# Optimization experiments

Hardware: AMD Instinct MI355X
Metric: run time of the kernel (lower is better)

The kernel has to match this reference:

```python
import jax, jax.numpy as jnp
from jax import lax
import numpy as np

_B, _D, _H, _W = 4, 32, 256, 256   # batch, sparse grid (z,y,x)
_NPER = 50000                      # active voxels per batch element
_EPS = 1e-3                        # BatchNorm eps from norm_fn


def _subm_rulebook(coords, D, H, W):
    # gather/scatter index pairs for a 3x3x3 submanifold conv (spconv rulebook)
    N = coords.shape[0]
    b, z, y, x = coords.T
    keys = ((b * D + z) * H + y) * W + x
    order = np.argsort(keys)
    sk = keys[order]
    rin, rout = [], []
    for dz in (-1, 0, 1):
        for dy in (-1, 0, 1):
            for dx in (-1, 0, 1):
                nz, ny, nx = z + dz, y + dy, x + dx
                valid = (nz >= 0) & (nz < D) & (ny >= 0) & (ny < H) & (nx >= 0) & (nx < W)
                qk = ((b * D + nz) * H + ny) * W + nx
                pos = np.clip(np.searchsorted(sk, qk), 0, N - 1)
                found = valid & (sk[pos] == qk)
                rin.append(order[pos[found]].astype(np.int32))
                rout.append(np.nonzero(found)[0].astype(np.int32))
    P = max(len(a) for a in rin)
    Ia = np.full((27, P), N, np.int32)   # sentinel N -> zero-padded row
    Oa = np.full((27, P), N, np.int32)
    for k in range(27):
        Ia[k, :len(rin[k])] = rin[k]
        Oa[k, :len(rout[k])] = rout[k]
    return Ia, Oa


def _build():
    rng = np.random.default_rng(0)
    coords = []
    for b in range(_B):
        lin = rng.choice(_D * _H * _W, _NPER, replace=False)
        z = lin // (_H * _W); y = (lin // _W) % _H; x = lin % _W
        coords.append(np.stack([np.full(_NPER, b), z, y, x], 1))
    coords = np.concatenate(coords).astype(np.int64)
    N = coords.shape[0]
    rb1_in, rb1_out = _subm_rulebook(coords, _D, _H, _W)
    # strided SparseConv3d (k=3, s=2, p=1) rulebook + output coord set
    Do, Ho, Wo = (_D - 1) // 2 + 1, (_H - 1) // 2 + 1, (_W - 1) // 2 + 1
    b, z, y, x = coords.T
    cin, ck, ckey = [], [], []
    k = 0
    for dz in range(3):
        for dy in range(3):
            for dx in range(3):
                oz2, oy2, ox2 = z + 1 - dz, y + 1 - dy, x + 1 - dx
                valid = (oz2 % 2 == 0) & (oy2 % 2 == 0) & (ox2 % 2 == 0)
                oz, oy, ox = oz2 // 2, oy2 // 2, ox2 // 2
                valid &= (oz >= 0) & (oz < Do) & (oy >= 0) & (oy < Ho) & (ox >= 0) & (ox < Wo)
                idx = np.nonzero(valid)[0]
                cin.append(idx)
                ck.append(np.full(len(idx), k))
                ckey.append(((b[idx] * Do + oz[idx]) * Ho + oy[idx]) * Wo + ox[idx])
                k += 1
    allkey = np.concatenate(ckey)
    ukeys, inv = np.unique(allkey, return_inverse=True)
    N2 = len(ukeys)
    cin = np.concatenate(cin); ck = np.concatenate(ck)
    Pd = max(int((ck == kk).sum()) for kk in range(27))
    Id = np.full((27, Pd), N, np.int32)
    Od = np.full((27, Pd), N2, np.int32)
    for kk in range(27):
        m = ck == kk; n = int(m.sum())
        Id[kk, :n] = cin[m]; Od[kk, :n] = inv[m]
    ox = ukeys % Wo; oy = (ukeys // Wo) % Ho
    oz = (ukeys // (Wo * Ho)) % Do; ob = ukeys // (Wo * Ho * Do)
    coords2 = np.stack([ob, oz, oy, ox], 1)
    rb2_in, rb2_out = _subm_rulebook(coords2, Do, Ho, Wo)
    return N, N2, rb1_in, rb1_out, Id, Od, rb2_in, rb2_out


def setup_inputs():
    N, N2, rb1_in, rb1_out, rbd_in, rbd_out, rb2_in, rb2_out = _build()
    ks = jax.random.split(jax.random.key(0), 8)
    Cin, C0, C1 = 5, 16, 32
    return dict(
        voxel_features=jax.random.normal(ks[0], (N, Cin), jnp.float32),
        W_in=jax.random.normal(ks[1], (27, Cin, C0), jnp.float32) * 0.1,
        g_in=jnp.ones(C0), b_in=jnp.zeros(C0),
        Wb1=jax.random.normal(ks[2], (2, 2, 27, C0, C0), jnp.float32) * 0.05,
        bb1=jnp.zeros((2, 2, C0)), gb1=jnp.ones((2, 2, C0)), beb1=jnp.zeros((2, 2, C0)),
        Wp=jax.random.normal(ks[3], (27, C0, 1), jnp.float32) * 0.05,
        Wd=jax.random.normal(ks[4], (27, C0, C1), jnp.float32) * 0.05,
        g_d=jnp.ones(C1), b_d=jnp.zeros(C1),
        Wb2=jax.random.normal(ks[5], (2, 2, 27, C1, C1), jnp.float32) * 0.05,
        bb2=jnp.zeros((2, 2, C1)), gb2=jnp.ones((2, 2, C1)), beb2=jnp.zeros((2, 2, C1)),
        rb1_in=jnp.asarray(rb1_in), rb1_out=jnp.asarray(rb1_out),
        rbd_in=jnp.asarray(rbd_in), rbd_out=jnp.asarray(rbd_out),
        rb2_in=jnp.asarray(rb2_in), rb2_out=jnp.asarray(rb2_out),
        n2=int(N2),
    )


def _sparse_conv(feat, W, rin, rout, nout):
    # rulebook gather-matmul-scatter; fixed 27-iteration loop over kernel offsets
    featp = jnp.concatenate([feat, jnp.zeros((1, feat.shape[1]), feat.dtype)], 0)
    out = jnp.zeros((nout + 1, W.shape[-1]), feat.dtype)
    for k in range(W.shape[0]):
        out = out.at[rout[k]].add(featp[rin[k]] @ W[k])
    return out[:nout]


def _bn(x, g, b):
    # training-mode BatchNorm1d over active voxels (eps=1e-3)
    m = x.mean(0)
    v = ((x - m) ** 2).mean(0)
    return g * (x - m) * lax.rsqrt(v + _EPS) + b


def _basic_block(feat, Wb, bb, gb, beb, rin, rout, n):
    out = _sparse_conv(feat, Wb[0], rin, rout, n) + bb[0]
    out = jax.nn.relu(_bn(out, gb[0], beb[0]))
    out = _sparse_conv(out, Wb[1], rin, rout, n) + bb[1]
    out = _bn(out, gb[1], beb[1])
    return jax.nn.relu(out + feat)


def _forward(voxel_features, W_in, g_in, b_in, Wb1, bb1, gb1, beb1, Wp, Wd, g_d, b_d,
             Wb2, bb2, gb2, beb2, rb1_in, rb1_out, rbd_in, rbd_out, rb2_in, rb2_out, n2):
    n1 = voxel_features.shape[0]
    # conv_input: SubMConv3d + BN + ReLU
    x = jax.nn.relu(_bn(_sparse_conv(voxel_features, W_in, rb1_in, rb1_out, n1), g_in, b_in))
    for i in range(2):
        x = _basic_block(x, Wb1[i], bb1[i], gb1[i], beb1[i], rb1_in, rb1_out, n1)
    # DynamicFocalPruningDownsample: learnable importance -> topk keep (1-0.5)
    imp = jax.nn.sigmoid(_sparse_conv(x, Wp, rb1_in, rb1_out, n1))[:, 0]
    x = x * imp[:, None]
    kkeep = n1 - n1 // 2
    kth = lax.top_k(imp, kkeep)[0][-1]
    x = jnp.where(imp[:, None] >= kth, x, jnp.zeros_like(x))
    # strided SparseConv3d 16->32 + BN + ReLU
    x2 = jax.nn.relu(_bn(_sparse_conv(x, Wd, rbd_in, rbd_out, n2), g_d, b_d))
    for i in range(2):
        x2 = _basic_block(x2, Wb2[i], bb2[i], gb2[i], beb2[i], rb2_in, rb2_out, n2)
    return x2


def reference(voxel_features, W_in, g_in, b_in, Wb1, bb1, gb1, beb1, Wp, Wd, g_d, b_d,
              Wb2, bb2, gb2, beb2, rb1_in, rb1_out, rbd_in, rbd_out, rb2_in, rb2_out, n2):
    return _forward(voxel_features, W_in, g_in, b_in, Wb1, bb1, gb1, beb1, Wp, Wd, g_d, b_d,
                    Wb2, bb2, gb2, beb2, rb1_in, rb1_out, rbd_in, rbd_out, rb2_in, rb2_out, n2)
```

## Files before the change

kernel.cpp:

```cpp
#include <hip/hip_runtime.h>


typedef __attribute__((ext_vector_type(8))) short bf16x8;
typedef __attribute__((ext_vector_type(4))) float f32x4;

static __device__ __forceinline__ unsigned f2bfu(float x) {
    unsigned b = __float_as_uint(x);
    return (b + 0x7FFFu + ((b >> 16) & 1u)) >> 16;
}

__global__ void rb_count_kernel(const int* __restrict__ rout, int P, int n_out,
                                int* __restrict__ cnt) {
    int k = threadIdx.x;
    if (k >= 27) return;
    const int* r = rout + (size_t)k * P;
    int lo = 0, hi = P;
    while (lo < hi) {
        int mid = (lo + hi) >> 1;
        if (r[mid] < n_out) lo = mid + 1; else hi = mid;
    }
    cnt[k] = lo;
}

__global__ void seg_build(const int* __restrict__ rout, const int* __restrict__ cnt,
                          int P, int nb, int gran, int* __restrict__ segs) {
    const int k = blockIdx.y;
    const int b = blockIdx.x * 256 + threadIdx.x;
    if (b > nb) return;
    const int target = b * gran;
    const int* r = rout + (size_t)k * P;
    int lo = 0, hi = cnt[k];
    while (lo < hi) {
        int m = (lo + hi) >> 1;
        if (r[m] < target) lo = m + 1; else hi = m;
    }
    segs[k * (nb + 1) + b] = lo;
}

__global__ void inv_build(const int* __restrict__ rin, const int* __restrict__ rout,
                          const int* __restrict__ cnt, int P, int n_out,
                          int* __restrict__ inv) {
    const int k = blockIdx.y;
    const int p = blockIdx.x * 256 + threadIdx.x;
    if (p < cnt[k])
        inv[(size_t)k * n_out + rout[(size_t)k * P + p]] = rin[(size_t)k * P + p];
}

__global__ void prepack_w(const float* __restrict__ W, int T, int CI, int S,
                          short* __restrict__ pack) {
    int idx = blockIdx.x * 256 + threadIdx.x;
    if (idx >= S * 128) return;
    int l = idx & 63, h = (idx >> 6) & 1, s = idx >> 7;
    int co = (l & 15) + 16 * h;
#pragma unroll
    for (int j = 0; j < 8; j++) {
        int gk = s * 32 + (l >> 4) * 8 + j;
        int tap = gk / CI, cin = gk % CI;
        float w = (tap < T) ? W[((size_t)tap * CI + cin) * 32 + co] : 0.f;
        pack[(size_t)idx * 8 + j] = (short)f2bfu(w);
    }
}

__global__ __launch_bounds__(256) void conv_mfma_sorted32(
        const float* __restrict__ feat, const short* __restrict__ Bp,
        const int* __restrict__ rin, const int* __restrict__ rout,
        const int* __restrict__ segs, int P, int nb16, int n_out,
        float* __restrict__ out, float* __restrict__ stats) {
    __shared__ int invw[64];
    __shared__ float part[2][4][32];
    const int t = threadIdx.x, wv = t >> 6, lane = t & 63;
    const int row = lane & 15, grp = lane >> 4;
    float ss0 = 0.f, qq0 = 0.f, ss1 = 0.f, qq1 = 0.f;

    for (int tile = 0; tile < 4; ++tile) {
        const int rowbase = blockIdx.x * 256 + wv * 64 + tile * 16;
        if (rowbase >= n_out) break;
        const int tix = rowbase >> 4;
        int segv = 0;
        if (lane < 28)      segv = segs[lane * (nb16 + 1) + tix];
        else if (lane < 56) segv = segs[(lane - 28) * (nb16 + 1) + tix + 1];
        f32x4 d0 = {0.f, 0.f, 0.f, 0.f}, d1 = {0.f, 0.f, 0.f, 0.f};
        for (int k = 0; k < 27; ++k) {
            const int s0 = __shfl(segv, k);
            const int s1 = __shfl(segv, 28 + k);
            if (s0 == s1) continue;
            if (lane < 16) invw[wv * 16 + lane] = -1;
            const int e = s0 + lane;
            if (lane < 16 && e < s1)
                invw[wv * 16 + (rout[(size_t)k * P + e] - rowbase)] = rin[(size_t)k * P + e];
            asm volatile("s_waitcnt lgkmcnt(0)" ::: "memory");
            const int rn = invw[wv * 16 + row];
            unsigned au0 = 0, au1 = 0, au2 = 0, au3 = 0;
            if (rn >= 0) {
                const float4 v0 = *(const float4*)(feat + (size_t)rn * 32 + grp * 8);
                const float4 v1 = *(const float4*)(feat + (size_t)rn * 32 + grp * 8 + 4);
                au0 = f2bfu(v0.x) | (f2bfu(v0.y) << 16);
                au1 = f2bfu(v0.z) | (f2bfu(v0.w) << 16);
                au2 = f2bfu(v1.x) | (f2bfu(v1.y) << 16);
                au3 = f2bfu(v1.z) | (f2bfu(v1.w) << 16);
            }
            union { unsigned u[4]; bf16x8 v; } ua;
            ua.u[0] = au0; ua.u[1] = au1; ua.u[2] = au2; ua.u[3] = au3;
            const bf16x8 b0 = *(const bf16x8*)(Bp + ((size_t)(2 * k) * 64 + lane) * 8);
            const bf16x8 b1 = *(const bf16x8*)(Bp + ((size_t)(2 * k + 1) * 64 + lane) * 8);
            d0 = __builtin_amdgcn_mfma_f32_16x16x32_bf16(ua.v, b0, d0, 0, 0, 0);
            d1 = __builtin_amdgcn_mfma_f32_16x16x32_bf16(ua.v, b1, d1, 0, 0, 0);
        }
        const int m0 = rowbase + grp * 4;
#pragma unroll
        for (int i = 0; i < 4; i++) {
            if (m0 + i < n_out) {
                out[(size_t)(m0 + i) * 32 + row]      = d0[i];
                out[(size_t)(m0 + i) * 32 + row + 16] = d1[i];
            }
            ss0 += d0[i]; qq0 += d0[i] * d0[i];
            ss1 += d1[i]; qq1 += d1[i] * d1[i];
        }
    }
#pragma unroll
    for (int d = 16; d <= 32; d <<= 1) {
        ss0 += __shfl_xor(ss0, d); qq0 += __shfl_xor(qq0, d);
        ss1 += __shfl_xor(ss1, d); qq1 += __shfl_xor(qq1, d);
    }
    if (lane < 16) {
        part[0][wv][row] = ss0; part[0][wv][row + 16] = ss1;
        part[1][wv][row] = qq0; part[1][wv][row + 16] = qq1;
    }
    __syncthreads();
    if (t < 64) {
        const int which = t >> 5, co = t & 31;
        atomicAdd(&stats[which * 32 + co],
                  part[which][0][co] + part[which][1][co] +
                  part[which][2][co] + part[which][3][co]);
    }
}

__global__ __launch_bounds__(256) void conv_mfma_inv16(
        const float* __restrict__ feat, const short* __restrict__ Bp,
        const int* __restrict__ inv, int n_out,
        float* __restrict__ out, float* __restrict__ stats) {
    __shared__ float part[2][4][32];
    const int t = threadIdx.x, wv = t >> 6, lane = t & 63;
    const int row = lane & 15, grp = lane >> 4;
    float ss0 = 0.f, qq0 = 0.f, ss1 = 0.f, qq1 = 0.f;

    for (int tile = 0; tile < 4; ++tile) {
        const int rowbase = blockIdx.x * 256 + wv * 64 + tile * 16;
        if (rowbase >= n_out) break;
        const int j = rowbase + row;
        f32x4 d0 = {0.f, 0.f, 0.f, 0.f}, d1 = {0.f, 0.f, 0.f, 0.f};
        for (int s = 0; s < 14; ++s) {
            const int tap = 2 * s + (grp >> 1);
            const int cin0 = (grp & 1) * 8;
            int rn = -1;
            if (tap < 27 && j < n_out) rn = inv[(size_t)tap * n_out + j];
            unsigned au0 = 0, au1 = 0, au2 = 0, au3 = 0;
            if (rn >= 0) {
                const float4 v0 = *(const float4*)(feat + (size_t)rn * 16 + cin0);
                const float4 v1 = *(const float4*)(feat + (size_t)rn * 16 + cin0 + 4);
                au0 = f2bfu(v0.x) | (f2bfu(v0.y) << 16);
                au1 = f2bfu(v0.z) | (f2bfu(v0.w) << 16);
                au2 = f2bfu(v1.x) | (f2bfu(v1.y) << 16);
                au3 = f2bfu(v1.z) | (f2bfu(v1.w) << 16);
            }
            union { unsigned u[4]; bf16x8 v; } ua;
            ua.u[0] = au0; ua.u[1] = au1; ua.u[2] = au2; ua.u[3] = au3;
            const bf16x8 b0 = *(const bf16x8*)(Bp + ((size_t)(2 * s) * 64 + lane) * 8);
            const bf16x8 b1 = *(const bf16x8*)(Bp + ((size_t)(2 * s + 1) * 64 + lane) * 8);
            d0 = __builtin_amdgcn_mfma_f32_16x16x32_bf16(ua.v, b0, d0, 0, 0, 0);
            d1 = __builtin_amdgcn_mfma_f32_16x16x32_bf16(ua.v, b1, d1, 0, 0, 0);
        }
        const int m0 = rowbase + grp * 4;
#pragma unroll
        for (int i = 0; i < 4; i++) {
            if (m0 + i < n_out) {
                out[(size_t)(m0 + i) * 32 + row]      = d0[i];
                out[(size_t)(m0 + i) * 32 + row + 16] = d1[i];
            }
            ss0 += d0[i]; qq0 += d0[i] * d0[i];
            ss1 += d1[i]; qq1 += d1[i] * d1[i];
        }
    }
#pragma unroll
    for (int d = 16; d <= 32; d <<= 1) {
        ss0 += __shfl_xor(ss0, d); qq0 += __shfl_xor(qq0, d);
        ss1 += __shfl_xor(ss1, d); qq1 += __shfl_xor(qq1, d);
    }
    if (lane < 16) {
        part[0][wv][row] = ss0; part[0][wv][row + 16] = ss1;
        part[1][wv][row] = qq0; part[1][wv][row + 16] = qq1;
    }
    __syncthreads();
    if (t < 64) {
        const int which = t >> 5, co = t & 31;
        atomicAdd(&stats[which * 32 + co],
                  part[which][0][co] + part[which][1][co] +
                  part[which][2][co] + part[which][3][co]);
    }
}

template <int COUT, bool SIGMOID, bool STATS>
__global__ __launch_bounds__(256) void conv16_wave(
        const float* __restrict__ feat, const float* __restrict__ W,
        const int* __restrict__ rin, const int* __restrict__ rout,
        const int* __restrict__ segs, int P, int nb64, int n_out,
        float* __restrict__ out, float* __restrict__ stats) {
    __shared__ int invw[4 * 64];
    __shared__ float part[2][4][COUT];
    const int t = threadIdx.x, wv = t >> 6, lane = t & 63;
    const int rowbase = blockIdx.x * 256 + wv * 64;
    const bool active = rowbase < n_out;
    float acc[COUT];
#pragma unroll
    for (int co = 0; co < COUT; co++) acc[co] = 0.f;

    if (active) {
        const int tix = rowbase >> 6;
        int segv = 0;
        if (lane < 28)      segv = segs[lane * (nb64 + 1) + tix];
        else if (lane < 56) segv = segs[(lane - 28) * (nb64 + 1) + tix + 1];
        for (int k = 0; k < 27; ++k) {
            const int s0 = __shfl(segv, k);
            const int s1 = __shfl(segv, 28 + k);
            if (s0 == s1) continue;
            invw[wv * 64 + lane] = -1;
            const int e = s0 + lane;
            if (e < s1)
                invw[wv * 64 + (rout[(size_t)k * P + e] - rowbase)] = rin[(size_t)k * P + e];
            asm volatile("s_waitcnt lgkmcnt(0)" ::: "memory");
            const int rn = invw[wv * 64 + lane];
            float f[16];
#pragma unroll
            for (int ci = 0; ci < 16; ci++) f[ci] = 0.f;
            if (rn >= 0) {
                const float* fr = feat + (size_t)rn * 16;
#pragma unroll
                for (int q = 0; q < 4; q++) {
                    const float4 v = *(const float4*)(fr + 4 * q);
                    f[4 * q] = v.x; f[4 * q + 1] = v.y;
                    f[4 * q + 2] = v.z; f[4 * q + 3] = v.w;
                }
            }
            const float* __restrict__ Wk = W + k * 16 * COUT;
#pragma unroll
            for (int ci = 0; ci < 16; ci++) {
                const float fv = f[ci];
#pragma unroll
                for (int co = 0; co < COUT; co++)
                    acc[co] = fmaf(fv, Wk[ci * COUT + co], acc[co]);
            }
        }
        const int j = rowbase + lane;
        if (j < n_out) {
#pragma unroll
            for (int co = 0; co < COUT; co++) {
                float v = acc[co];
                if (SIGMOID) v = 1.f / (1.f + expf(-v));
                out[(size_t)j * COUT + co] = v;
            }
        }
    }
    if (STATS) {
#pragma unroll
        for (int co = 0; co < COUT; co++) {
            float s = acc[co], s2 = s * s;
#pragma unroll
            for (int d = 1; d < 64; d <<= 1) {
                s += __shfl_xor(s, d);
                s2 += __shfl_xor(s2, d);
            }
            if (lane == 0) { part[0][wv][co] = s; part[1][wv][co] = s2; }
        }
        __syncthreads();
        if (t < 2 * COUT) {
            const int which = t / COUT, co = t - which * COUT;
            atomicAdd(&stats[which * COUT + co],
                      part[which][0][co] + part[which][1][co] +
                      part[which][2][co] + part[which][3][co]);
        }
    }
}

template <int CIN, int COUT>
__global__ __launch_bounds__(256) void conv_gather(
        const float* __restrict__ feat, const float* __restrict__ W,
        const int* __restrict__ rin, const int* __restrict__ rout,
        const int* __restrict__ segs, int P, int n_out,
        float* __restrict__ out, float* __restrict__ stats) {
    __shared__ int2 invl[256];
    __shared__ int seg[54];
    __shared__ float part[2][4][COUT];
    const int t = threadIdx.x;
    const int j0 = blockIdx.x * 256;
    const int nb1 = gridDim.x + 1;
    if (t < 54) seg[t] = segs[(t >> 1) * nb1 + blockIdx.x + (t & 1)];
    invl[t] = make_int2(-1, -1);
    float acc[COUT];
#pragma unroll
    for (int co = 0; co < COUT; co++) acc[co] = 0.f;
    __syncthreads();

    for (int k = 0; k < 27; k++) {
        const int s0 = seg[2 * k], s1 = seg[2 * k + 1];
        if (s0 == s1) continue;
        const int idx = s0 + t;
        if (idx < s1)
            invl[rout[(size_t)k * P + idx] - j0] = make_int2(k, rin[(size_t)k * P + idx]);
        __syncthreads();
        const int2 e = invl[t];
        const int in = (e.x == k) ? e.y : -1;
        __syncthreads();

        float f[CIN];
#pragma unroll
        for (int ci = 0; ci < CIN; ci++) f[ci] = 0.f;
        if (in >= 0) {
            const float* fr = feat + (size_t)in * CIN;
#pragma unroll
            for (int ci = 0; ci < CIN; ci++) f[ci] = fr[ci];
        }
        const float* __restrict__ Wk = W + k * CIN * COUT;
#pragma unroll
        for (int ci = 0; ci < CIN; ci++) {
            const float fv = f[ci];
#pragma unroll
            for (int co = 0; co < COUT; co++)
                acc[co] = fmaf(fv, Wk[ci * COUT + co], acc[co]);
        }
    }

    const int j = j0 + t;
    if (j < n_out) {
#pragma unroll
        for (int co = 0; co < COUT; co++) out[(size_t)j * COUT + co] = acc[co];
    }
    const int wv = t >> 6, lane = t & 63;
#pragma unroll
    for (int co = 0; co < COUT; co++) {
        float s = acc[co], s2 = s * s;
#pragma unroll
        for (int d = 1; d < 64; d <<= 1) {
            s += __shfl_xor(s, d);
            s2 += __shfl_xor(s2, d);
        }
        if (lane == 0) { part[0][wv][co] = s; part[1][wv][co] = s2; }
    }
    __syncthreads();
    if (t < 2 * COUT) {
        const int which = t / COUT, co = t - which * COUT;
        atomicAdd(&stats[which * COUT + co],
                  part[which][0][co] + part[which][1][co] +
                  part[which][2][co] + part[which][3][co]);
    }
}

template <int C, bool RELU>
__global__ void bn_apply(const float* __restrict__ x, const float* __restrict__ stats,
                         const float* __restrict__ gg, const float* __restrict__ bb,
                         int n, float* __restrict__ y) {
    const float nf = (float)n;
    const long long total = (long long)n * C;
    for (long long idx = (long long)blockIdx.x * blockDim.x + threadIdx.x;
         idx < total; idx += (long long)gridDim.x * blockDim.x) {
        int ch = (int)(idx & (C - 1));
        float m = stats[ch] / nf;
        float v = stats[C + ch] / nf - m * m;
        float r = rsqrtf(v + 1e-3f);
        float val = gg[ch] * (x[idx] - m) * r + bb[ch];
        if (RELU) val = fmaxf(val, 0.f);
        y[idx] = val;
    }
}

template <int C>
__global__ void bn_apply_addrelu(const float* __restrict__ x,
                                 const float* __restrict__ skip,
                                 const float* __restrict__ stats,
                                 const float* __restrict__ gg,
                                 const float* __restrict__ bb,
                                 int n, float* __restrict__ y) {
    const float nf = (float)n;
    const long long total = (long long)n * C;
    for (long long idx = (long long)blockIdx.x * blockDim.x + threadIdx.x;
         idx < total; idx += (long long)gridDim.x * blockDim.x) {
        int ch = (int)(idx & (C - 1));
        float m = stats[ch] / nf;
        float v = stats[C + ch] / nf - m * m;
        float r = rsqrtf(v + 1e-3f);
        float val = gg[ch] * (x[idx] - m) * r + bb[ch] + skip[idx];
        y[idx] = fmaxf(val, 0.f);
    }
}

__global__ __launch_bounds__(256) void hist_pass(const float* __restrict__ imp, int n,
                                                 int pass, const int* __restrict__ state,
                                                 int* __restrict__ hist) {
    __shared__ int lh[256];
    const int t = threadIdx.x;
    lh[t] = 0;
    __syncthreads();
    const int shift = 24 - 8 * pass;
    unsigned prefix = 0;
    if (pass > 0) prefix = (unsigned)state[0];
    for (int i = blockIdx.x * 256 + t; i < n; i += gridDim.x * 256) {
        unsigned u = __float_as_uint(imp[i]);
        if (pass == 0 || (u >> (shift + 8)) == prefix)
            atomicAdd(&lh[(u >> shift) & 0xFFu], 1);
    }
    __syncthreads();
    if (lh[t]) atomicAdd(&hist[pass * 256 + t], lh[t]);
}

__global__ __launch_bounds__(256) void scan_byte(const int* __restrict__ hist,
                                                 int kkeep, int pass,
                                                 int* __restrict__ state) {
    __shared__ int h[256];
    const int t = threadIdx.x;
    h[t] = hist[pass * 256 + t];
    __syncthreads();
    if (t == 0) {
        const int target = (pass == 0) ? kkeep : state[1];
        int acc = 0; int b = 255;
        for (; b > 0; b--) {
            if (acc + h[b] >= target) break;
            acc += h[b];
        }
        unsigned prefix = (pass == 0) ? 0u : (unsigned)state[0];
        prefix = (prefix << 8) | (unsigned)b;
        state[0] = (int)prefix;
        state[1] = target - acc;
        if (pass == 3) state[2] = (int)prefix;
    }
}

__global__ void prune_mask(float* __restrict__ x, const float* __restrict__ imp,
                           const int* __restrict__ state, int n) {
    const unsigned K = (unsigned)state[2];
    int i = blockIdx.x * blockDim.x + threadIdx.x;
    if (i >= n) return;
    float im = imp[i];
    float mult = (__float_as_uint(im) >= K) ? im : 0.f;
#pragma unroll
    for (int c = 0; c < 16; c++) x[(size_t)i * 16 + c] *= mult;
}

extern "C" void kernel_launch(void* const* d_in, const int* in_sizes, int n_in,
                              void* d_out, int out_size, void* d_ws, size_t ws_size,
                              hipStream_t stream) {
    const float* vf    = (const float*)d_in[0];
    const float* W_in  = (const float*)d_in[1];
    const float* g_in  = (const float*)d_in[2];
    const float* b_in  = (const float*)d_in[3];
    const float* Wb1   = (const float*)d_in[4];
    const float* gb1   = (const float*)d_in[6];
    const float* beb1  = (const float*)d_in[7];
    const float* Wp    = (const float*)d_in[8];
    const float* Wd    = (const float*)d_in[9];
    const float* g_d   = (const float*)d_in[10];
    const float* b_d   = (const float*)d_in[11];
    const float* Wb2   = (const float*)d_in[12];
    const float* gb2   = (const float*)d_in[14];
    const float* beb2  = (const float*)d_in[15];
    const int* rb1_in  = (const int*)d_in[16];
    const int* rb1_out = (const int*)d_in[17];
    const int* rbd_in  = (const int*)d_in[18];
    const int* rbd_out = (const int*)d_in[19];
    const int* rb2_in  = (const int*)d_in[20];
    const int* rb2_out = (const int*)d_in[21];

    const int N  = in_sizes[0] / 5;
    const int P1 = in_sizes[16] / 27;
    const int Pd = in_sizes[18] / 27;
    const int P2 = in_sizes[20] / 27;
    const int n2 = out_size / 32;
    const int kkeep = N - N / 2;

    const int gs1   = (N + 255) / 256;
    const int gm2   = (n2 + 255) / 256;
    const int nb16  = (n2 + 15) / 16;
    const int nb64  = (N + 63) / 64;
    const int gew   = 2048;

    auto pad4 = [](size_t v) { return (v + 3) & ~(size_t)3; };
    float* A     = (float*)d_ws;
    float* B     = A   + pad4((size_t)N * 16);
    float* imp   = B   + pad4((size_t)N * 16);
    float* D     = imp + pad4((size_t)N);
    float* E     = D   + pad4((size_t)n2 * 32);
    float* stats = E   + pad4((size_t)n2 * 32);
    int*   cnt1  = (int*)(stats + 64);
    int*   cntd  = cnt1 + 32;
    int*   cnt2  = cntd + 32;
    int*   hist4 = cnt2 + 32;
    int*   state = hist4 + 1024;
    int*   segs1 = state + 8;
    int*   segs64 = segs1 + 27 * (gs1 + 1);
    int*   invd   = (int*)E;
    int*   segs16 = (int*)B;
    short* pack2  = (short*)imp;
    short* packd  = pack2 + 4 * 27648;
    float* OUT   = (float*)d_out;
    float* C2    = OUT;

    rb_count_kernel<<<1, 32, 0, stream>>>(rb1_out, P1, N,  cnt1);
    rb_count_kernel<<<1, 32, 0, stream>>>(rbd_out, Pd, n2, cntd);
    rb_count_kernel<<<1, 32, 0, stream>>>(rb2_out, P2, n2, cnt2);
    seg_build<<<dim3((gs1 + 256) / 256, 27), 256, 0, stream>>>(rb1_out, cnt1, P1, gs1, 256, segs1);
    seg_build<<<dim3((nb64 + 256) / 256, 27), 256, 0, stream>>>(rb1_out, cnt1, P1, nb64, 64, segs64);

    hipMemsetAsync(stats, 0, 64 * 4, stream);
    conv_gather<5, 16><<<gs1, 256, 0, stream>>>(vf, W_in, rb1_in, rb1_out, segs1, P1, N, B, stats);
    bn_apply<16, true><<<gew, 256, 0, stream>>>(B, stats, g_in, b_in, N, A);

    for (int i = 0; i < 2; i++) {
        const float* W0 = Wb1 + (size_t)(i * 2 + 0) * 27 * 256;
        const float* W1 = Wb1 + (size_t)(i * 2 + 1) * 27 * 256;
        hipMemsetAsync(stats, 0, 64 * 4, stream);
        conv16_wave<16, false, true><<<gs1, 256, 0, stream>>>(A, W0, rb1_in, rb1_out, segs64, P1, nb64, N, B, stats);
        bn_apply<16, true><<<gew, 256, 0, stream>>>(B, stats, gb1 + (i * 2 + 0) * 16, beb1 + (i * 2 + 0) * 16, N, B);
        hipMemsetAsync(stats, 0, 64 * 4, stream);
        conv16_wave<16, false, true><<<gs1, 256, 0, stream>>>(B, W1, rb1_in, rb1_out, segs64, P1, nb64, N, C2, stats);
        bn_apply_addrelu<16><<<gew, 256, 0, stream>>>(C2, A, stats, gb1 + (i * 2 + 1) * 16, beb1 + (i * 2 + 1) * 16, N, A);
    }

    conv16_wave<1, true, false><<<gs1, 256, 0, stream>>>(A, Wp, rb1_in, rb1_out, segs64, P1, nb64, N, imp, stats);
    hipMemsetAsync(hist4, 0, 1024 * 4, stream);
    for (int p = 0; p < 4; p++) {
        hist_pass<<<128, 256, 0, stream>>>(imp, N, p, state, hist4);
        scan_byte<<<1, 256, 0, stream>>>(hist4, kkeep, p, state);
    }
    prune_mask<<<(N + 255) / 256, 256, 0, stream>>>(A, imp, state, N);

    seg_build<<<dim3((nb16 + 256) / 256, 27), 256, 0, stream>>>(rb2_out, cnt2, P2, nb16, 16, segs16);
    for (int w = 0; w < 4; w++)
        prepack_w<<<14, 256, 0, stream>>>(Wb2 + (size_t)w * 27 * 1024, 27, 32, 27, pack2 + (size_t)w * 27648);
    prepack_w<<<7, 256, 0, stream>>>(Wd, 27, 16, 14, packd);
    hipMemsetAsync(invd, 0xFF, (size_t)27 * n2 * 4, stream);
    inv_build<<<dim3((Pd + 255) / 256, 27), 256, 0, stream>>>(rbd_in, rbd_out, cntd, Pd, n2, invd);

    hipMemsetAsync(stats, 0, 64 * 4, stream);
    conv_mfma_inv16<<<gm2, 256, 0, stream>>>(A, packd, invd, n2, D, stats);
    bn_apply<32, true><<<gew, 256, 0, stream>>>(D, stats, g_d, b_d, n2, D);

    for (int i = 0; i < 2; i++) {
        const short* P0 = pack2 + (size_t)(i * 2 + 0) * 27648;
        const short* P1w = pack2 + (size_t)(i * 2 + 1) * 27648;
        hipMemsetAsync(stats, 0, 64 * 4, stream);
        conv_mfma_sorted32<<<gm2, 256, 0, stream>>>(D, P0, rb2_in, rb2_out, segs16, P2, nb16, n2, E, stats);
        bn_apply<32, true><<<gew, 256, 0, stream>>>(E, stats, gb2 + (i * 2 + 0) * 32, beb2 + (i * 2 + 0) * 32, n2, E);
        hipMemsetAsync(stats, 0, 64 * 4, stream);
        conv_mfma_sorted32<<<gm2, 256, 0, stream>>>(E, P1w, rb2_in, rb2_out, segs16, P2, nb16, n2, OUT, stats);
        bn_apply_addrelu<32><<<gew, 256, 0, stream>>>(OUT, D, stats, gb2 + (i * 2 + 1) * 32, beb2 + (i * 2 + 1) * 32, n2, (i == 0) ? D : OUT);
    }
}
```

Baseline: 1.522 ms.

## Store stage-2 activations in bf16 and swizzle block order across XCDs

After: 1.282 ms. -15.8%, faster.

```diff
diff --git a/kernel.cpp b/kernel.cpp
--- a/kernel.cpp
+++ b/kernel.cpp
@@ -7,6 +7,15 @@
 static __device__ __forceinline__ unsigned f2bfu(float x) {
     unsigned b = __float_as_uint(x);
     return (b + 0x7FFFu + ((b >> 16) & 1u)) >> 16;
+}
+static __device__ __forceinline__ float bf2f(unsigned short u) {
+    return __uint_as_float(((unsigned)u) << 16);
+}
+static __device__ __forceinline__ int xcd_swz(int bid, int nwg) {
+    if (nwg < 16) return bid;
+    int q = nwg >> 3, r = nwg & 7;
+    int x = bid & 7, i = bid >> 3;
+    return (x < r ? x * (q + 1) : r * (q + 1) + (x - r) * q) + i;
 }
 
 __global__ void rb_count_kernel(const int* __restrict__ rout, int P, int n_out,
@@ -61,19 +70,21 @@
     }
 }
 
+template <bool OUT_BF16>
 __global__ __launch_bounds__(256) void conv_mfma_sorted32(
-        const float* __restrict__ feat, const short* __restrict__ Bp,
+        const unsigned short* __restrict__ feat, const short* __restrict__ Bp,
         const int* __restrict__ rin, const int* __restrict__ rout,
         const int* __restrict__ segs, int P, int nb16, int n_out,
-        float* __restrict__ out, float* __restrict__ stats) {
+        void* __restrict__ outv, float* __restrict__ stats) {
     __shared__ int invw[64];
     __shared__ float part[2][4][32];
     const int t = threadIdx.x, wv = t >> 6, lane = t & 63;
     const int row = lane & 15, grp = lane >> 4;
+    const int bid = xcd_swz(blockIdx.x, gridDim.x);
     float ss0 = 0.f, qq0 = 0.f, ss1 = 0.f, qq1 = 0.f;
 
     for (int tile = 0; tile < 4; ++tile) {
-        const int rowbase = blockIdx.x * 256 + wv * 64 + tile * 16;
+        const int rowbase = bid * 256 + wv * 64 + tile * 16;
         if (rowbase >= n_out) break;
         const int tix = rowbase >> 4;
         int segv = 0;
@@ -90,17 +101,10 @@
                 invw[wv * 16 + (rout[(size_t)k * P + e] - rowbase)] = rin[(size_t)k * P + e];
             asm volatile("s_waitcnt lgkmcnt(0)" ::: "memory");
             const int rn = invw[wv * 16 + row];
-            unsigned au0 = 0, au1 = 0, au2 = 0, au3 = 0;
-            if (rn >= 0) {
-                const float4 v0 = *(const float4*)(feat + (size_t)rn * 32 + grp * 8);
-                const float4 v1 = *(const float4*)(feat + (size_t)rn * 32 + grp * 8 + 4);
-                au0 = f2bfu(v0.x) | (f2bfu(v0.y) << 16);
-                au1 = f2bfu(v0.z) | (f2bfu(v0.w) << 16);
-                au2 = f2bfu(v1.x) | (f2bfu(v1.y) << 16);
-                au3 = f2bfu(v1.z) | (f2bfu(v1.w) << 16);
-            }
-            union { unsigned u[4]; bf16x8 v; } ua;
-            ua.u[0] = au0; ua.u[1] = au1; ua.u[2] = au2; ua.u[3] = au3;
+            union { int u[4]; bf16x8 v; } ua;
+            ua.u[0] = ua.u[1] = ua.u[2] = ua.u[3] = 0;
+            if (rn >= 0)
+                ua.v = *(const bf16x8*)(feat + (size_t)rn * 32 + grp * 8);
             const bf16x8 b0 = *(const bf16x8*)(Bp + ((size_t)(2 * k) * 64 + lane) * 8);
             const bf16x8 b1 = *(const bf16x8*)(Bp + ((size_t)(2 * k + 1) * 64 + lane) * 8);
             d0 = __builtin_amdgcn_mfma_f32_16x16x32_bf16(ua.v, b0, d0, 0, 0, 0);
@@ -110,8 +114,15 @@
 #pragma unroll
         for (int i = 0; i < 4; i++) {
             if (m0 + i < n_out) {
-                out[(size_t)(m0 + i) * 32 + row]      = d0[i];
-                out[(size_t)(m0 + i) * 32 + row + 16] = d1[i];
+                if (OUT_BF16) {
+                    unsigned short* o = (unsigned short*)outv;
+                    o[(size_t)(m0 + i) * 32 + row]      = (unsigned short)f2bfu(d0[i]);
+                    o[(size_t)(m0 + i) * 32 + row + 16] = (unsigned short)f2bfu(d1[i]);
+                } else {
+                    float* o = (float*)outv;
+                    o[(size_t)(m0 + i) * 32 + row]      = d0[i];
+                    o[(size_t)(m0 + i) * 32 + row + 16] = d1[i];
+                }
             }
             ss0 += d0[i]; qq0 += d0[i] * d0[i];
             ss1 += d1[i]; qq1 += d1[i] * d1[i];
@@ -136,16 +147,17 @@
 }
 
 __global__ __launch_bounds__(256) void conv_mfma_inv16(
-        const float* __restrict__ feat, const short* __restrict__ Bp,
+        const unsigned short* __restrict__ feat, const short* __restrict__ Bp,
         const int* __restrict__ inv, int n_out,
-        float* __restrict__ out, float* __restrict__ stats) {
+        unsigned short* __restrict__ out, float* __restrict__ stats) {
     __shared__ float part[2][4][32];
     const int t = threadIdx.x, wv = t >> 6, lane = t & 63;
     const int row = lane & 15, grp = lane >> 4;
+    const int bid = xcd_swz(blockIdx.x, gridDim.x);
     float ss0 = 0.f, qq0 = 0.f, ss1 = 0.f, qq1 = 0.f;
 
     for (int tile = 0; tile < 4; ++tile) {
-        const int rowbase = blockIdx.x * 256 + wv * 64 + tile * 16;
+        const int rowbase = bid * 256 + wv * 64 + tile * 16;
         if (rowbase >= n_out) break;
         const int j = rowbase + row;
         f32x4 d0 = {0.f, 0.f, 0.f, 0.f}, d1 = {0.f, 0.f, 0.f, 0.f};
@@ -154,17 +166,10 @@
             const int cin0 = (grp & 1) * 8;
             int rn = -1;
             if (tap < 27 && j < n_out) rn = inv[(size_t)tap * n_out + j];
-            unsigned au0 = 0, au1 = 0, au2 = 0, au3 = 0;
-            if (rn >= 0) {
-                const float4 v0 = *(const float4*)(feat + (size_t)rn * 16 + cin0);
-                const float4 v1 = *(const float4*)(feat + (size_t)rn * 16 + cin0 + 4);
-                au0 = f2bfu(v0.x) | (f2bfu(v0.y) << 16);
-                au1 = f2bfu(v0.z) | (f2bfu(v0.w) << 16);
-                au2 = f2bfu(v1.x) | (f2bfu(v1.y) << 16);
-                au3 = f2bfu(v1.z) | (f2bfu(v1.w) << 16);
-            }
-            union { unsigned u[4]; bf16x8 v; } ua;
-            ua.u[0] = au0; ua.u[1] = au1; ua.u[2] = au2; ua.u[3] = au3;
+            union { int u[4]; bf16x8 v; } ua;
+            ua.u[0] = ua.u[1] = ua.u[2] = ua.u[3] = 0;
+            if (rn >= 0)
+                ua.v = *(const bf16x8*)(feat + (size_t)rn * 16 + cin0);
             const bf16x8 b0 = *(const bf16x8*)(Bp + ((size_t)(2 * s) * 64 + lane) * 8);
             const bf16x8 b1 = *(const bf16x8*)(Bp + ((size_t)(2 * s + 1) * 64 + lane) * 8);
             d0 = __builtin_amdgcn_mfma_f32_16x16x32_bf16(ua.v, b0, d0, 0, 0, 0);
@@ -174,8 +179,8 @@
 #pragma unroll
         for (int i = 0; i < 4; i++) {
             if (m0 + i < n_out) {
-                out[(size_t)(m0 + i) * 32 + row]      = d0[i];
-                out[(size_t)(m0 + i) * 32 + row + 16] = d1[i];
+                out[(size_t)(m0 + i) * 32 + row]      = (unsigned short)f2bfu(d0[i]);
+                out[(size_t)(m0 + i) * 32 + row + 16] = (unsigned short)f2bfu(d1[i]);
             }
             ss0 += d0[i]; qq0 += d0[i] * d0[i];
             ss1 += d1[i]; qq1 += d1[i] * d1[i];
@@ -208,7 +213,8 @@
     __shared__ int invw[4 * 64];
     __shared__ float part[2][4][COUT];
     const int t = threadIdx.x, wv = t >> 6, lane = t & 63;
-    const int rowbase = blockIdx.x * 256 + wv * 64;
+    const int bid = xcd_swz(blockIdx.x, gridDim.x);
+    const int rowbase = bid * 256 + wv * 64;
     const bool active = rowbase < n_out;
     float acc[COUT];
 #pragma unroll
@@ -291,9 +297,10 @@
     __shared__ int seg[54];
     __shared__ float part[2][4][COUT];
     const int t = threadIdx.x;
-    const int j0 = blockIdx.x * 256;
+    const int bid = xcd_swz(blockIdx.x, gridDim.x);
+    const int j0 = bid * 256;
     const int nb1 = gridDim.x + 1;
-    if (t < 54) seg[t] = segs[(t >> 1) * nb1 + blockIdx.x + (t & 1)];
+    if (t < 54) seg[t] = segs[(t >> 1) * nb1 + bid + (t & 1)];
     invl[t] = make_int2(-1, -1);
     float acc[COUT];
 #pragma unroll
@@ -392,6 +399,47 @@
     }
 }
 
+template <int C>
+__global__ void bn_apply_b(const unsigned short* __restrict__ x,
+                           const float* __restrict__ stats,
+                           const float* __restrict__ gg, const float* __restrict__ bb,
+                           int n, unsigned short* __restrict__ y) {
+    const float nf = (float)n;
+    const long long total = (long long)n * C;
+    for (long long idx = (long long)blockIdx.x * blockDim.x + threadIdx.x;
+         idx < total; idx += (long long)gridDim.x * blockDim.x) {
+        int ch = (int)(idx & (C - 1));
+        float m = stats[ch] / nf;
+        float v = stats[C + ch] / nf - m * m;
+        float r = rsqrtf(v + 1e-3f);
+        float val = gg[ch] * (bf2f(x[idx]) - m) * r + bb[ch];
+        val = fmaxf(val, 0.f);
+        y[idx] = (unsigned short)f2bfu(val);
+    }
+}
+
+template <int C, bool OUT_BF16>
+__global__ void bn_addrelu_sb(const float* __restrict__ x,
+                              const unsigned short* __restrict__ skip,
+                              const float* __restrict__ stats,
+                              const float* __restrict__ gg,
+                              const float* __restrict__ bb,
+                              int n, void* __restrict__ yv) {
+    const float nf = (float)n;
+    const long long total = (long long)n * C;
+    for (long long idx = (long long)blockIdx.x * blockDim.x + threadIdx.x;
+         idx < total; idx += (long long)gridDim.x * blockDim.x) {
+        int ch = (int)(idx & (C - 1));
+        float m = stats[ch] / nf;
+        float v = stats[C + ch] / nf - m * m;
+        float r = rsqrtf(v + 1e-3f);
+        float val = gg[ch] * (x[idx] - m) * r + bb[ch] + bf2f(skip[idx]);
+        val = fmaxf(val, 0.f);
+        if (OUT_BF16) ((unsigned short*)yv)[idx] = (unsigned short)f2bfu(val);
+        else          ((float*)yv)[idx] = val;
+    }
+}
+
 __global__ __launch_bounds__(256) void hist_pass(const float* __restrict__ imp, int n,
                                                  int pass, const int* __restrict__ state,
                                                  int* __restrict__ hist) {
@@ -433,15 +481,17 @@
     }
 }
 
-__global__ void prune_mask(float* __restrict__ x, const float* __restrict__ imp,
-                           const int* __restrict__ state, int n) {
+__global__ void prune_mask_ab(const float* __restrict__ x, const float* __restrict__ imp,
+                              const int* __restrict__ state, int n,
+                              unsigned short* __restrict__ ab) {
     const unsigned K = (unsigned)state[2];
     int i = blockIdx.x * blockDim.x + threadIdx.x;
     if (i >= n) return;
     float im = imp[i];
     float mult = (__float_as_uint(im) >= K) ? im : 0.f;
 #pragma unroll
-    for (int c = 0; c < 16; c++) x[(size_t)i * 16 + c] *= mult;
+    for (int c = 0; c < 16; c++)
+        ab[(size_t)i * 16 + c] = (unsigned short)f2bfu(x[(size_t)i * 16 + c] * mult);
 }
 
 extern "C" void kernel_launch(void* const* d_in, const int* in_sizes, int n_in,
@@ -485,9 +535,10 @@
     float* A     = (float*)d_ws;
     float* B     = A   + pad4((size_t)N * 16);
     float* imp   = B   + pad4((size_t)N * 16);
-    float* D     = imp + pad4((size_t)N);
-    float* E     = D   + pad4((size_t)n2 * 32);
-    float* stats = E   + pad4((size_t)n2 * 32);
+    float* FI    = imp + pad4((size_t)N);
+    float* Dbf   = FI  + pad4((size_t)n2 * 32);
+    float* Ebf   = Dbf + pad4((size_t)n2 * 16);
+    float* stats = Ebf + pad4((size_t)n2 * 16);
     int*   cnt1  = (int*)(stats + 64);
     int*   cntd  = cnt1 + 32;
     int*   cnt2  = cntd + 32;
@@ -495,10 +546,14 @@
     int*   state = hist4 + 1024;
     int*   segs1 = state + 8;
     int*   segs64 = segs1 + 27 * (gs1 + 1);
-    int*   invd   = (int*)E;
-    int*   segs16 = (int*)B;
+    int*   invd   = (int*)FI;
+    float* F      = FI;
+    unsigned short* Ab = (unsigned short*)B;
+    int*   segs16 = (int*)(B + pad4((size_t)N * 8));
     short* pack2  = (short*)imp;
     short* packd  = pack2 + 4 * 27648;
+    unsigned short* Db = (unsigned short*)Dbf;
+    unsigned short* Eb = (unsigned short*)Ebf;
     float* OUT   = (float*)d_out;
     float* C2    = OUT;
 
@@ -529,7 +584,7 @@
         hist_pass<<<128, 256, 0, stream>>>(imp, N, p, state, hist4);
         scan_byte<<<1, 256, 0, stream>>>(hist4, kkeep, p, state);
     }
-    prune_mask<<<(N + 255) / 256, 256, 0, stream>>>(A, imp, state, N);
+    prune_mask_ab<<<(N + 255) / 256, 256, 0, stream>>>(A, imp, state, N, Ab);
 
     seg_build<<<dim3((nb16 + 256) / 256, 27), 256, 0, stream>>>(rb2_out, cnt2, P2, nb16, 16, segs16);
     for (int w = 0; w < 4; w++)
@@ -539,17 +594,20 @@
     inv_build<<<dim3((Pd + 255) / 256, 27), 256, 0, stream>>>(rbd_in, rbd_out, cntd, Pd, n2, invd);
 
     hipMemsetAsync(stats, 0, 64 * 4, stream);
-    conv_mfma_inv16<<<gm2, 256, 0, stream>>>(A, packd, invd, n2, D, stats);
-    bn_apply<32, true><<<gew, 256, 0, stream>>>(D, stats, g_d, b_d, n2, D);
+    conv_mfma_inv16<<<gm2, 256, 0, stream>>>(Ab, packd, invd, n2, Db, stats);
+    bn_apply_b<32><<<gew, 256, 0, stream>>>(Db, stats, g_d, b_d, n2, Db);
 
     for (int i = 0; i < 2; i++) {
         const short* P0 = pack2 + (size_t)(i * 2 + 0) * 27648;
         const short* P1w = pack2 + (size_t)(i * 2 + 1) * 27648;
         hipMemsetAsync(stats, 0, 64 * 4, stream);
-        conv_mfma_sorted32<<<gm2, 256, 0, stream>>>(D, P0, rb2_in, rb2_out, segs16, P2, nb16, n2, E, stats);
-        bn_apply<32, true><<<gew, 256, 0, stream>>>(E, stats, gb2 + (i * 2 + 0) * 32, beb2 + (i * 2 + 0) * 32, n2, E);
+        conv_mfma_sorted32<true><<<gm2, 256, 0, stream>>>(Db, P0, rb2_in, rb2_out, segs16, P2, nb16, n2, Eb, stats);
+        bn_apply_b<32><<<gew, 256, 0, stream>>>(Eb, stats, gb2 + (i * 2 + 0) * 32, beb2 + (i * 2 + 0) * 32, n2, Eb);
         hipMemsetAsync(stats, 0, 64 * 4, stream);
-        conv_mfma_sorted32<<<gm2, 256, 0, stream>>>(E, P1w, rb2_in, rb2_out, segs16, P2, nb16, n2, OUT, stats);
-        bn_apply_addrelu<32><<<gew, 256, 0, stream>>>(OUT, D, stats, gb2 + (i * 2 + 1) * 32, beb2 + (i * 2 + 1) * 32, n2, (i == 0) ? D : OUT);
-    }
-}
+        conv_mfma_sorted32<false><<<gm2, 256, 0, stream>>>(Eb, P1w, rb2_in, rb2_out, segs16, P2, nb16, n2, F, stats);
+        if (i == 0)
+            bn_addrelu_sb<32, true><<<gew, 256, 0, stream>>>(F, Db, stats, gb2 + 32, beb2 + 32, n2, Db);
+        else
+            bn_addrelu_sb<32, false><<<gew, 256, 0, stream>>>(F, Db, stats, gb2 + 96, beb2 + 96, n2, OUT);
+    }
+}
```
